# Performance work log

Measured on AMD Instinct MI355X. Metric: run time of the kernel, lower is better.

Reference implementation:

```python
import jax, jax.numpy as jnp
import numpy as np

WINDOW = 128  # crop size (compute_crops default window_size)


def centre_crop(centroids, window_size, h, w):
    # centroids: [C,2] int; returns flat gather coords [2, C*ws*ws]
    half = window_size // 2
    cy = jnp.clip(centroids[:, 0], half, h - half)
    cx = jnp.clip(centroids[:, 1], half, w - half)
    gy, gx = jnp.meshgrid(jnp.arange(window_size), jnp.arange(window_size), indexing='ij')
    rows = (cy - half)[:, None, None] + gy[None]  # [C,ws,ws]
    cols = (cx - half)[:, None, None] + gx[None]
    return jnp.stack([rows.reshape(-1), cols.reshape(-1)])  # [2, C*ws*ws]


def setup_inputs() -> dict:
    key = jax.random.key(0)
    ks = jax.random.split(key, 8)
    E, S, C, H, W = 6, 1, 512, 1024, 1024
    Dh = 16
    return {
        'x': jax.random.normal(ks[0], (E, H, W), dtype=jnp.float32),
        'sigma': jax.random.uniform(ks[1], (S, H, W), dtype=jnp.float32),
        'c': jax.random.normal(ks[2], (C, E), dtype=jnp.float32),
        'W1': jax.random.normal(ks[3], (E + S, Dh), dtype=jnp.float32) * 0.3,
        'b1': jnp.zeros((Dh,), dtype=jnp.float32),
        'W2': jax.random.normal(ks[4], (Dh, Dh), dtype=jnp.float32) * 0.3,
        'b2': jnp.zeros((Dh,), dtype=jnp.float32),
        'W3': jax.random.normal(ks[5], (Dh, 1), dtype=jnp.float32) * 0.3,
        'b3': jnp.zeros((1,), dtype=jnp.float32),
        'centroids_idx': jax.random.randint(ks[6], (C, 2), 0, H, dtype=jnp.int32),
    }


def reference(x, sigma, c, W1, b1, W2, b2, W3, b3, centroids_idx):
    E, h, w = x.shape
    S = sigma.shape[0]
    C = c.shape[0]
    ws = WINDOW
    mesh = centre_crop(centroids_idx, ws, h, w)  # [2, C*ws*ws]
    # gather per-instance windows from concatenated embedding+sigma maps
    xs = jnp.concatenate([x, sigma], axis=0)  # [E+S, H, W]
    g = xs[:, mesh[0], mesh[1]]               # [E+S, C*ws*ws]
    g = g.reshape(E + S, C, ws, ws).transpose(1, 0, 2, 3)  # [C, E+S, ws, ws]
    # subtract centroid descriptor from embedding channels (feature_engineering '0')
    g = jnp.concatenate([g[:, :E] - c[:, :, None, None], g[:, E:]], axis=1)
    feats = g.transpose(0, 2, 3, 1).reshape(-1, E + S)  # [(C*ws*ws), E+S]
    # per-pixel probability MLP (ProbabilityNet)
    hdn = jax.nn.relu(feats @ W1 + b1)
    hdn = jax.nn.relu(hdn @ W2 + b2)
    prob = jax.nn.sigmoid(hdn @ W3 + b3)
    prob = prob.reshape(C, 1, ws, ws)
    # instance-id / coordinate table for the downstream scatter (iidd)
    inst = jnp.repeat(jnp.arange(C, dtype=mesh.dtype), ws * ws)
    iidd = jnp.concatenate([inst[None], mesh], axis=0)  # [3, C*ws*ws]
    return prob, iidd
```

## Files before the change

kernel.cpp:

```cpp
#include <hip/hip_runtime.h>

#define WS 128
#define HW (1024 * 1024)
#define PLANE 8388608

typedef _Float16 half4 __attribute__((ext_vector_type(4)));
typedef _Float16 half8 __attribute__((ext_vector_type(8)));
typedef float floatx4 __attribute__((ext_vector_type(4)));

__global__ __launch_bounds__(256) void precompute_G(
    const float* __restrict__ x,
    const float* __restrict__ sigma,
    _Float16* __restrict__ G)
{
    const int px = blockIdx.x * 256 + threadIdx.x;
    half8 g;
#pragma unroll
    for (int e = 0; e < 6; ++e) g[e] = (_Float16)x[e * HW + px];
    g[6] = (_Float16)sigma[px];
    g[7] = (_Float16)0.0f;
    *(half8*)(G + (size_t)px * 8) = g;
}

__global__ __launch_bounds__(256) void instanseg_mlp(
    const _Float16* __restrict__ G,
    const float* __restrict__ c,
    const float* __restrict__ W1,
    const float* __restrict__ b1,
    const float* __restrict__ W2,
    const float* __restrict__ b2,
    const float* __restrict__ W3,
    const float* __restrict__ b3,
    const int*   __restrict__ cent,
    float* __restrict__ out)
{
    const int cid  = blockIdx.y;
    const int lane = threadIdx.x & 63;
    const int wave = threadIdx.x >> 6;
    const int quad = lane >> 4;
    const int sub  = lane & 15;

    const int cy = min(max(cent[2 * cid], 64), 960);
    const int cx = min(max(cent[2 * cid + 1], 64), 960);
    const int cy0 = cy - 64, cx0 = cx - 64;

    half4 a1;
#pragma unroll
    for (int i = 0; i < 4; ++i) {
        const int k = 4 * quad + i;
        a1[i] = (k < 7) ? (_Float16)W1[k * 16 + sub] : (_Float16)0.0f;
    }

    half4 a2;
    float w3f[4], bb2[4], qf[4];
#pragma unroll
    for (int i = 0; i < 4; ++i) {
        const int k = 4 * quad + i;
        a2[i]  = (_Float16)W2[k * 16 + sub];
        w3f[i] = W3[k];
        bb2[i] = b2[k];
        float qv = -b1[k];
#pragma unroll
        for (int e = 0; e < 6; ++e)
            qv = fmaf(W1[e * 16 + k], c[cid * 6 + e], qv);
        qf[i] = qv;
    }
    const float b3v = b3[0];
    const floatx4 zero = {0.0f, 0.0f, 0.0f, 0.0f};

    const int wavestart = blockIdx.x * 2048 + wave * 512;

    for (int it = 0; it < 8; ++it) {
        const int start = wavestart + it * 64;
        float logit[4];
#pragma unroll
        for (int ch = 0; ch < 4; ++ch) {
            const int gp  = start + ch * 16 + sub;
            const int src = (cy0 + (gp >> 7)) * 1024 + cx0 + (gp & 127);

            half4 bg = {};
            if (quad < 2)
                bg = *(const half4*)(G + (size_t)src * 8 + quad * 4);

            floatx4 c1 = __builtin_amdgcn_mfma_f32_16x16x16f16(a1, bg, zero, 0, 0, 0);

            half4 h;
#pragma unroll
            for (int i = 0; i < 4; ++i)
                h[i] = (_Float16)fmaxf(c1[i] - qf[i], 0.0f);

            floatx4 c2 = __builtin_amdgcn_mfma_f32_16x16x16f16(a2, h, zero, 0, 0, 0);

            float part = 0.0f;
#pragma unroll
            for (int i = 0; i < 4; ++i)
                part = fmaf(w3f[i], fmaxf(c2[i] + bb2[i], 0.0f), part);
            part += __shfl_xor(part, 16, 64);
            part += __shfl_xor(part, 32, 64);
            logit[ch] = part;
        }

        const float l01 = (quad & 1) ? logit[1] : logit[0];
        const float l23 = (quad & 1) ? logit[3] : logit[2];
        const float lg  = (quad & 2) ? l23 : l01;
        const float prob = 1.0f / (1.0f + __expf(-(lg + b3v)));

        const int gps = start + lane;
        const int n   = cid * 16384 + gps;
        out[n]             = prob;
        out[PLANE + n]     = (float)cid;
        out[2 * PLANE + n] = (float)(cy0 + (gps >> 7));
        out[3 * PLANE + n] = (float)(cx0 + (gps & 127));
    }
}

extern "C" void kernel_launch(void* const* d_in, const int* in_sizes, int n_in,
                              void* d_out, int out_size, void* d_ws, size_t ws_size,
                              hipStream_t stream) {
    const float* x     = (const float*)d_in[0];
    const float* sigma = (const float*)d_in[1];
    const float* c     = (const float*)d_in[2];
    const float* W1    = (const float*)d_in[3];
    const float* b1    = (const float*)d_in[4];
    const float* W2    = (const float*)d_in[5];
    const float* b2    = (const float*)d_in[6];
    const float* W3    = (const float*)d_in[7];
    const float* b3    = (const float*)d_in[8];
    const int*   cent  = (const int*)d_in[9];
    float* out = (float*)d_out;
    _Float16* G = (_Float16*)d_ws;

    precompute_G<<<dim3(HW / 256), dim3(256), 0, stream>>>(x, sigma, G);
    instanseg_mlp<<<dim3(8, 512), dim3(256), 0, stream>>>(
        G, c, W1, b1, W2, b2, W3, b3, cent, out);
}
```

Baseline: 201.0 us.

## Fuse fp16 packing into per-row kernel staging image rows in LDS

Removes the separate precompute kernel and its global fp16 staging buffer. Each block now handles one image row: it converts that row into LDS, builds a list of crops whose window covers the row, and runs the MFMA MLP for every covering crop straight from LDS. Bias terms move into the MFMA accumulator inputs. Gathers from global memory and one launch go away, but work per row is uneven because rows near popular centroids carry many more crops, and the per-block atomic list adds overhead.

```diff
diff --git a/kernel.cpp b/kernel.cpp
--- a/kernel.cpp
+++ b/kernel.cpp
@@ -1,6 +1,5 @@
 #include <hip/hip_runtime.h>
 
-#define WS 128
 #define HW (1024 * 1024)
 #define PLANE 8388608
 
@@ -8,22 +7,9 @@
 typedef _Float16 half8 __attribute__((ext_vector_type(8)));
 typedef float floatx4 __attribute__((ext_vector_type(4)));
 
-__global__ __launch_bounds__(256) void precompute_G(
+__global__ __launch_bounds__(256) void instanseg_row(
     const float* __restrict__ x,
     const float* __restrict__ sigma,
-    _Float16* __restrict__ G)
-{
-    const int px = blockIdx.x * 256 + threadIdx.x;
-    half8 g;
-#pragma unroll
-    for (int e = 0; e < 6; ++e) g[e] = (_Float16)x[e * HW + px];
-    g[6] = (_Float16)sigma[px];
-    g[7] = (_Float16)0.0f;
-    *(half8*)(G + (size_t)px * 8) = g;
-}
-
-__global__ __launch_bounds__(256) void instanseg_mlp(
-    const _Float16* __restrict__ G,
     const float* __restrict__ c,
     const float* __restrict__ W1,
     const float* __restrict__ b1,
@@ -34,83 +20,113 @@
     const int*   __restrict__ cent,
     float* __restrict__ out)
 {
-    const int cid  = blockIdx.y;
-    const int lane = threadIdx.x & 63;
-    const int wave = threadIdx.x >> 6;
-    const int quad = lane >> 4;
-    const int sub  = lane & 15;
+    __shared__ _Float16 rowG[1024 * 8];
+    __shared__ float    cs[512 * 6];
+    __shared__ int      centS[1024];
+    __shared__ int      wlist[512];
+    __shared__ int      wcount;
 
-    const int cy = min(max(cent[2 * cid], 64), 960);
-    const int cx = min(max(cent[2 * cid + 1], 64), 960);
-    const int cy0 = cy - 64, cx0 = cx - 64;
+    const int y   = blockIdx.x;
+    const int tid = threadIdx.x;
 
-    half4 a1;
+    if (tid == 0) wcount = 0;
+
+    for (int i = tid; i < 1024; i += 256) centS[i] = cent[i];
+    for (int i = tid; i < 3072; i += 256) cs[i] = c[i];
+
+#pragma unroll
+    for (int p4 = 0; p4 < 4; ++p4) {
+        const int px = p4 * 256 + tid;
+        half8 g;
+#pragma unroll
+        for (int e = 0; e < 6; ++e) g[e] = (_Float16)x[e * HW + y * 1024 + px];
+        g[6] = (_Float16)sigma[y * 1024 + px];
+        g[7] = (_Float16)0.0f;
+        *(half8*)&rowG[px * 8] = g;
+    }
+    __syncthreads();
+
+    for (int w = tid; w < 512; w += 256) {
+        const int cy0 = min(max(centS[2 * w], 64), 960) - 64;
+        if (y >= cy0 && y < cy0 + 128)
+            wlist[atomicAdd(&wcount, 1)] = w;
+    }
+    __syncthreads();
+    const int nw = wcount;
+    if (nw == 0) return;
+
+    const int lane = tid & 63, wave = tid >> 6;
+    const int quad = lane >> 4, sub = lane & 15;
+
+    half4 a1, a2;
+    float w3f[4], b1r[4], w1n[6][4];
+    floatx4 cb;
 #pragma unroll
     for (int i = 0; i < 4; ++i) {
         const int k = 4 * quad + i;
-        a1[i] = (k < 7) ? (_Float16)W1[k * 16 + sub] : (_Float16)0.0f;
-    }
-
-    half4 a2;
-    float w3f[4], bb2[4], qf[4];
-#pragma unroll
-    for (int i = 0; i < 4; ++i) {
-        const int k = 4 * quad + i;
+        a1[i]  = (k < 7) ? (_Float16)W1[k * 16 + sub] : (_Float16)0.0f;
         a2[i]  = (_Float16)W2[k * 16 + sub];
         w3f[i] = W3[k];
-        bb2[i] = b2[k];
-        float qv = -b1[k];
+        cb[i]  = b2[k];
+        b1r[i] = b1[k];
 #pragma unroll
-        for (int e = 0; e < 6; ++e)
-            qv = fmaf(W1[e * 16 + k], c[cid * 6 + e], qv);
-        qf[i] = qv;
+        for (int e = 0; e < 6; ++e) w1n[e][i] = W1[e * 16 + k];
     }
     const float b3v = b3[0];
-    const floatx4 zero = {0.0f, 0.0f, 0.0f, 0.0f};
 
-    const int wavestart = blockIdx.x * 2048 + wave * 512;
+    for (int wi = wave; wi < nw; wi += 4) {
+        const int cid = wlist[wi];
+        const int cy0 = min(max(centS[2 * cid], 64), 960) - 64;
+        const int cx0 = min(max(centS[2 * cid + 1], 64), 960) - 64;
 
-    for (int it = 0; it < 8; ++it) {
-        const int start = wavestart + it * 64;
-        float logit[4];
+        floatx4 cq;
 #pragma unroll
-        for (int ch = 0; ch < 4; ++ch) {
-            const int gp  = start + ch * 16 + sub;
-            const int src = (cy0 + (gp >> 7)) * 1024 + cx0 + (gp & 127);
-
-            half4 bg = {};
-            if (quad < 2)
-                bg = *(const half4*)(G + (size_t)src * 8 + quad * 4);
-
-            floatx4 c1 = __builtin_amdgcn_mfma_f32_16x16x16f16(a1, bg, zero, 0, 0, 0);
-
-            half4 h;
+        for (int i = 0; i < 4; ++i) {
+            float qv = b1r[i];
 #pragma unroll
-            for (int i = 0; i < 4; ++i)
-                h[i] = (_Float16)fmaxf(c1[i] - qf[i], 0.0f);
-
-            floatx4 c2 = __builtin_amdgcn_mfma_f32_16x16x16f16(a2, h, zero, 0, 0, 0);
-
-            float part = 0.0f;
-#pragma unroll
-            for (int i = 0; i < 4; ++i)
-                part = fmaf(w3f[i], fmaxf(c2[i] + bb2[i], 0.0f), part);
-            part += __shfl_xor(part, 16, 64);
-            part += __shfl_xor(part, 32, 64);
-            logit[ch] = part;
+            for (int e = 0; e < 6; ++e)
+                qv = fmaf(-w1n[e][i], cs[cid * 6 + e], qv);
+            cq[i] = qv;
         }
 
-        const float l01 = (quad & 1) ? logit[1] : logit[0];
-        const float l23 = (quad & 1) ? logit[3] : logit[2];
-        const float lg  = (quad & 2) ? l23 : l01;
-        const float prob = 1.0f / (1.0f + __expf(-(lg + b3v)));
+        const int orow = (y - cy0) * 128;
 
-        const int gps = start + lane;
-        const int n   = cid * 16384 + gps;
-        out[n]             = prob;
-        out[PLANE + n]     = (float)cid;
-        out[2 * PLANE + n] = (float)(cy0 + (gps >> 7));
-        out[3 * PLANE + n] = (float)(cx0 + (gps & 127));
+#pragma unroll
+        for (int f = 0; f < 2; ++f) {
+            float logit[4];
+#pragma unroll
+            for (int ch = 0; ch < 4; ++ch) {
+                half4 v = (half4)(_Float16)0.0f;
+                if (quad < 2)
+                    v = *(const half4*)&rowG[(cx0 + f * 64 + ch * 16 + sub) * 8 + quad * 4];
+
+                floatx4 c1 = __builtin_amdgcn_mfma_f32_16x16x16f16(a1, v, cq, 0, 0, 0);
+                half4 h;
+#pragma unroll
+                for (int i = 0; i < 4; ++i)
+                    h[i] = (_Float16)fmaxf(c1[i], 0.0f);
+                floatx4 c2 = __builtin_amdgcn_mfma_f32_16x16x16f16(a2, h, cb, 0, 0, 0);
+
+                float part = 0.0f;
+#pragma unroll
+                for (int i = 0; i < 4; ++i)
+                    part = fmaf(w3f[i], fmaxf(c2[i], 0.0f), part);
+                part += __shfl_xor(part, 16, 64);
+                part += __shfl_xor(part, 32, 64);
+                logit[ch] = part;
+            }
+
+            const float l01 = (quad & 1) ? logit[1] : logit[0];
+            const float l23 = (quad & 1) ? logit[3] : logit[2];
+            const float lg  = (quad & 2) ? l23 : l01;
+            const float prob = 1.0f / (1.0f + __expf(-(lg + b3v)));
+
+            const int n = cid * 16384 + orow + f * 64 + lane;
+            out[n]             = prob;
+            out[PLANE + n]     = (float)cid;
+            out[2 * PLANE + n] = (float)y;
+            out[3 * PLANE + n] = (float)(cx0 + f * 64 + lane);
+        }
     }
 }
 
@@ -128,9 +144,8 @@
     const float* b3    = (const float*)d_in[8];
     const int*   cent  = (const int*)d_in[9];
     float* out = (float*)d_out;
-    _Float16* G = (_Float16*)d_ws;
+    (void)d_ws; (void)ws_size;
 
-    precompute_G<<<dim3(HW / 256), dim3(256), 0, stream>>>(x, sigma, G);
-    instanseg_mlp<<<dim3(8, 512), dim3(256), 0, stream>>>(
-        G, c, W1, b1, W2, b2, W3, b3, cent, out);
+    instanseg_row<<<dim3(1024), dim3(256), 0, stream>>>(
+        x, sigma, c, W1, b1, W2, b2, W3, b3, cent, out);
 }
```

After: 210.9 us. +4.9%, slower.
